# Performance work log

Measured on AMD Instinct MI355X. Metric: run time of the kernel, lower is better.

## Reference

```python
import jax, jax.numpy as jnp
import numpy as np

# ---- dims (from init_kwargs) ----
B_SZ = 16; K = 1; NC = 64; NR = 4; RF = 4; L_UL = 8
M_ANT = 256; N_ANT = 1024; BS_TDD = 16; RIS_TDD = 16
FC = 100e9; BW = 1e9; UPSNR = 10.0; MAX_DELAY = 5e-9; BIT = 1
C = NC  # PSA channel = Nc


def setup_inputs():
    key = jax.random.key(0)
    ks = jax.random.split(key, 20)
    f = jnp.float32
    d = {}
    d['H_BR_re'] = jax.random.normal(ks[0], (NC, N_ANT, M_ANT), f)
    d['H_BR_im'] = jax.random.normal(ks[1], (NC, N_ANT, M_ANT), f)
    d['H_RU_re'] = jax.random.normal(ks[2], (B_SZ, K, NC, NR, N_ANT), f)
    d['H_RU_im'] = jax.random.normal(ks[3], (B_SZ, K, NC, NR, N_ANT), f)
    d['H_BU_re'] = jax.random.normal(ks[4], (B_SZ, K, NC, NR, M_ANT), f)
    d['H_BU_im'] = jax.random.normal(ks[5], (B_SZ, K, NC, NR, M_ANT), f)
    # unit complex Gaussian noise, scaled by sqrt(Power*SNR/2) inside reference
    d['noise_re'] = jax.random.normal(ks[6], (B_SZ, L_UL, NC, NR, RF), f)
    d['noise_im'] = jax.random.normal(ks[7], (B_SZ, L_UL, NC, NR, RF), f)
    # learned parameters (torch: Parameter tensors in __init__)
    d['Phase1'] = jax.random.uniform(ks[8], (L_UL, N_ANT), f)
    d['Phase2'] = jax.random.uniform(ks[9], (L_UL, N_ANT), f)
    d['Phase_TDD'] = jax.random.normal(ks[10], (L_UL, RIS_TDD), f)
    d['S_analog'] = jax.random.normal(ks[11], (L_UL, NC, M_ANT, RF), f)
    d['S_analog_TDD'] = jax.random.normal(ks[12], (L_UL, NC, BS_TDD, RF), f)
    # ParallelPolarizedSelfAttention(channel=Nc) weights (1x1 convs -> [out,in])
    s = 0.05
    d['ch_wv_w'] = jax.random.normal(ks[13], (C // 2, C), f) * s
    d['ch_wv_b'] = jnp.zeros((C // 2,), f)
    d['ch_wq_w'] = jax.random.normal(ks[14], (1, C), f) * s
    d['ch_wq_b'] = jnp.zeros((1,), f)
    d['ch_wz_w'] = jax.random.normal(ks[15], (C, C // 2), f) * s
    d['ch_wz_b'] = jnp.zeros((C,), f)
    d['ln_w'] = jnp.ones((C,), f)
    d['ln_b'] = jnp.zeros((C,), f)
    d['sp_wv_w'] = jax.random.normal(ks[16], (C // 2, C), f) * s
    d['sp_wv_b'] = jnp.zeros((C // 2,), f)
    d['sp_wq_w'] = jax.random.normal(ks[17], (C // 2, C), f) * s
    d['sp_wq_b'] = jnp.zeros((C // 2,), f)
    return d


def _conv1x1(x, w, b):
    # 1x1 conv == channel mixing
    return jnp.einsum('bchw,oc->bohw', x, w) + b[None, :, None, None]


def _psa(x, ch_wv_w, ch_wv_b, ch_wq_w, ch_wq_b, ch_wz_w, ch_wz_b, ln_w, ln_b,
         sp_wv_w, sp_wv_b, sp_wq_w, sp_wq_b):
    # Parallel Polarized Self-Attention (channel branch + spatial branch)
    b, c, h, w = x.shape
    # channel-only self-attention
    cwv = _conv1x1(x, ch_wv_w, ch_wv_b).reshape(b, c // 2, h * w)
    cwq = jax.nn.softmax(_conv1x1(x, ch_wq_w, ch_wq_b).reshape(b, h * w), axis=1)
    cwz = jnp.einsum('bkn,bn->bk', cwv, cwq)          # [b, c//2]
    z = cwz @ ch_wz_w.T + ch_wz_b                      # [b, c]
    mu = jnp.mean(z, axis=-1, keepdims=True)
    var = jnp.var(z, axis=-1, keepdims=True)
    zn = (z - mu) / jnp.sqrt(var + 1e-5) * ln_w + ln_b  # LayerNorm over channel
    ch_weight = jax.nn.sigmoid(zn)[:, :, None, None]
    # spatial-only self-attention
    swv = _conv1x1(x, sp_wv_w, sp_wv_b).reshape(b, c // 2, h * w)
    swq = jax.nn.softmax(jnp.mean(_conv1x1(x, sp_wq_w, sp_wq_b), axis=(2, 3)), axis=-1)
    swz = jnp.einsum('bk,bkn->bn', swq, swv)
    sp_weight = jax.nn.sigmoid(swz.reshape(b, 1, h, w))
    return sp_weight * x + ch_weight * x


def reference(H_BR_re, H_BR_im, H_RU_re, H_RU_im, H_BU_re, H_BU_im,
              noise_re, noise_im, Phase1, Phase2, Phase_TDD, S_analog, S_analog_TDD,
              ch_wv_w, ch_wv_b, ch_wq_w, ch_wq_b, ch_wz_w, ch_wz_b, ln_w, ln_b,
              sp_wv_w, sp_wv_b, sp_wq_w, sp_wq_b):
    H_BR = H_BR_re + 1j * H_BR_im                       # [Nc, N_ant, M_ant]
    H_RU = H_RU_re[:, K - 1] + 1j * H_RU_im[:, K - 1]   # [B, Nc, Nr, N_ant]
    H_BU = H_BU_re[:, K - 1] + 1j * H_BU_im[:, K - 1]   # [B, Nc, Nr, M_ant]
    two_pi = 2.0 * jnp.pi
    # subcarrier frequencies fm = (n - (Nc+1)/2) * B/Nc + fc
    fm = ((jnp.arange(NC, dtype=jnp.float32) + 1.0) - (NC + 1) / 2.0) * (BW / NC) + FC
    # phase quantization (bit = 1 -> seg = pi)
    seg = two_pi / (2 ** BIT)
    th1 = jnp.exp(1j * (jnp.floor(two_pi * Phase1 / seg) * seg))  # [L, N_ant]
    th2 = jnp.exp(1j * (jnp.floor(two_pi * Phase2 / seg) * seg))  # [L, N_ant]
    # RIS true-time-delay phase, kron(Phi_T, ones(1, N_ant//RIS_TDD)) == repeat
    a1 = MAX_DELAY * jax.nn.sigmoid(Phase_TDD)                    # [L, RIS_TDD]
    phi_t = jnp.exp(1j * two_pi * fm[None, :, None] * a1[:, None, :])
    phi_tdd = jnp.repeat(phi_t, N_ANT // RIS_TDD, axis=-1)        # [L, Nc, N_ant]
    theta = th1[:, None, :] * phi_tdd * th2[:, None, :]           # diag(Theta) entries
    # BS analog precoder with TTDs; kron(S_T, ones(M//BS_TDD,1)) == row repeat
    S = jnp.exp(1j * S_analog) / float(np.sqrt(M_ANT))            # [L, Nc, M, RF]
    bdel = MAX_DELAY * jax.nn.sigmoid(S_analog_TDD)               # [L, Nc, BS_TDD, RF]
    s_t = jnp.exp(1j * two_pi * fm[None, :, None, None] * bdel)
    F = S * jnp.repeat(s_t, M_ANT // BS_TDD, axis=2)              # [L, Nc, M, RF]
    # H_RU @ diag(theta) == column-wise scaling (fused, no NxN diag matmul)
    scaled = H_RU[:, None] * theta[None, :, :, None, :]           # [B, L, Nc, Nr, N_ant]
    a = jnp.einsum('blcrn,cnm->blcrm', scaled, H_BR) + H_BU[:, None]
    y0 = jnp.einsum('blcrm,lcmf->blcrf', a, F)                    # [B, L, Nc, Nr, RF]
    power = jnp.sum(jnp.abs(y0) ** 2, axis=(3, 4))[..., None, None]
    snr_lin = 10.0 ** (-UPSNR / 10.0)
    noise = (noise_re + 1j * noise_im) * jnp.sqrt(power * snr_lin / 2.0)
    y = y0 + noise
    Y = jnp.transpose(y, (0, 2, 3, 4, 1)).reshape(B_SZ, NC, K * NR * RF, L_UL)
    x = jnp.concatenate([jnp.real(Y), jnp.imag(Y)], axis=3)       # [B, Nc, K*Nr*RF, 2L]
    return _psa(x, ch_wv_w, ch_wv_b, ch_wq_w, ch_wq_b, ch_wz_w, ch_wz_b,
                ln_w, ln_b, sp_wv_w, sp_wv_b, sp_wq_w, sp_wq_b)
```

## Files before the change

kernel.cpp:

```cpp
#include <hip/hip_runtime.h>
#include <math.h>

static constexpr double TWO_PI_D = 6.283185307179586476925287;

static constexpr size_t OFF_THRE = 0;
static constexpr size_t OFF_THIM = 524288;
static constexpr size_t OFF_FBF  = 1048576;
static constexpr size_t OFF_WTBF = 1572864;
static constexpr size_t OFF_Y0P  = 3670016;
static constexpr size_t OFF_X    = 4980736;
static constexpr size_t WS_FLOATS = 5242880;

typedef __attribute__((ext_vector_type(8))) short short8;
typedef __attribute__((ext_vector_type(4))) float f32x4;
typedef __attribute__((address_space(3))) unsigned int lds_u32;
typedef const __attribute__((address_space(1))) unsigned int glo_u32;

__device__ __forceinline__ double fm_of(int c){
  return ((double)(c + 1) - 32.5) * (1.0e9 / 64.0) + 1.0e11;
}
__device__ __forceinline__ unsigned short f2bf(float x){
  unsigned int u = __float_as_uint(x);
  return (unsigned short)((u + 0x7FFFu + ((u >> 16) & 1u)) >> 16);
}

__global__ __launch_bounds__(256) void k_prep(
    const float* __restrict__ P1, const float* __restrict__ P2,
    const float* __restrict__ PT, const float* __restrict__ SA,
    const float* __restrict__ ST,
    float* __restrict__ tre, float* __restrict__ tim, unsigned short* __restrict__ Fbf)
{
  __shared__ double tcs[16], tsn[16];
  int bid = blockIdx.x, tid = threadIdx.x;
  const float TWO_PI_F = 6.2831855f, SEG_F = 3.1415927f;
  if (bid < 2048){
    int l = bid >> 8, c = (bid >> 2) & 63, n0 = (bid & 3) * 256;
    if (tid < 4){
      int ris = (n0 >> 6) + tid;
      double a1 = 5.0e-9 / (1.0 + exp((double)(-PT[l * 16 + ris])));
      sincos(TWO_PI_D * fm_of(c) * a1, &tsn[tid], &tcs[tid]);
    }
    __syncthreads();
    int n = n0 + tid;
    float p1 = P1[l * 1024 + n], p2 = P2[l * 1024 + n];
    int k1 = (int)floorf((TWO_PI_F * p1) / SEG_F);
    int k2 = (int)floorf((TWO_PI_F * p2) / SEG_F);
    float s = ((k1 + k2) & 1) ? -1.f : 1.f;
    int t = (l * 64 + c) * 1024 + n;
    int ti = tid >> 6;
    tre[t] = s * (float)tcs[ti];
    tim[t] = s * (float)tsn[ti];
  } else {
    int bid2 = bid - 2048;
    int l = bid2 >> 8, c = (bid2 >> 2) & 63, f = bid2 & 3;
    int m = tid;
    if (tid < 16){
      double bdel = 5.0e-9 / (1.0 + exp((double)(-ST[((l * 64 + c) * 16 + tid) * 4 + f])));
      sincos(TWO_PI_D * fm_of(c) * bdel, &tsn[tid], &tcs[tid]);
    }
    __syncthreads();
    float sa_ = SA[(size_t)((l * 64 + c) * 256 + m) * 4 + f];
    float ssa, csa;
    sincosf(sa_, &ssa, &csa);
    float cb = (float)tcs[m >> 4], sb = (float)tsn[m >> 4];
    size_t base = ((size_t)(c * 2) * 32 + (l * 4 + f)) * 256 + m;
    Fbf[base]        = f2bf((csa * cb - ssa * sb) * 0.0625f);
    Fbf[base + 8192] = f2bf((csa * sb + ssa * cb) * 0.0625f);
  }
}

__global__ __launch_bounds__(256, 2) void k_W(
    const float* __restrict__ Hre, const float* __restrict__ Him,
    const unsigned short* __restrict__ Fbf,
    const float* __restrict__ tre, const float* __restrict__ tim,
    unsigned short* __restrict__ WTbf)
{
  __shared__ __align__(16) float lA[16640];
  const int bid = blockIdx.x;
  const int c = bid >> 5;
  const int n0 = (bid & 31) * 32;
  const int tid = threadIdx.x;
  const int lane = tid & 63, w = tid >> 6;

  const float* hre0 = Hre + ((size_t)c * 1024 + n0) * 256;
  const float* him0 = Him + ((size_t)c * 1024 + n0) * 256;
  #pragma unroll
  for (int i = 0; i < 16; i++){
    int t = w * 16 + i;
    int row = t & 31;
    const float* src = ((t >> 5) ? him0 : hre0) + (size_t)row * 256 + (lane << 2);
    __builtin_amdgcn_global_load_lds((glo_u32*)src, (lds_u32*)&lA[t * 260], 16, 0, 0);
  }
  __syncthreads();

  const int lftile = w & 1, rowhalf = w >> 1;
  const int kq = lane >> 4, rm = lane & 15;
  const int lf = lftile * 16 + rm;
  const int rrow = rowhalf * 16 + rm;
  const int nt = n0 + rowhalf * 16;

  const float* aRe = &lA[rrow * 260 + kq * 8];
  const float* aIm = aRe + 32 * 260;
  const unsigned short* fr = Fbf + (size_t)c * 16384 + (size_t)lf * 256 + kq * 8;
  const unsigned short* fi = fr + 8192;

  f32x4 accRe = {0.f,0.f,0.f,0.f}, accIm = {0.f,0.f,0.f,0.f};

  #pragma unroll
  for (int ck = 0; ck < 8; ck++){
    const int mo = ck * 32;
    float4 r0 = *(const float4*)(aRe + mo);
    float4 r1 = *(const float4*)(aRe + mo + 4);
    float4 i0 = *(const float4*)(aIm + mo);
    float4 i1 = *(const float4*)(aIm + mo + 4);
    short8 bre = *(const short8*)(fr + mo);
    short8 bim = *(const short8*)(fi + mo);
    short8 are, aim, bin;
    are[0]=(short)f2bf(r0.x); are[1]=(short)f2bf(r0.y); are[2]=(short)f2bf(r0.z); are[3]=(short)f2bf(r0.w);
    are[4]=(short)f2bf(r1.x); are[5]=(short)f2bf(r1.y); are[6]=(short)f2bf(r1.z); are[7]=(short)f2bf(r1.w);
    aim[0]=(short)f2bf(i0.x); aim[1]=(short)f2bf(i0.y); aim[2]=(short)f2bf(i0.z); aim[3]=(short)f2bf(i0.w);
    aim[4]=(short)f2bf(i1.x); aim[5]=(short)f2bf(i1.y); aim[6]=(short)f2bf(i1.z); aim[7]=(short)f2bf(i1.w);
    #pragma unroll
    for (int j = 0; j < 8; j++) bin[j] = bim[j] ^ (short)0x8000;
    accRe = __builtin_amdgcn_mfma_f32_16x16x32_bf16(are, bre, accRe, 0, 0, 0);
    accRe = __builtin_amdgcn_mfma_f32_16x16x32_bf16(aim, bin, accRe, 0, 0, 0);
    accIm = __builtin_amdgcn_mfma_f32_16x16x32_bf16(are, bim, accIm, 0, 0, 0);
    accIm = __builtin_amdgcn_mfma_f32_16x16x32_bf16(aim, bre, accIm, 0, 0, 0);
  }

  {
    const int l = lf >> 2;
    unsigned short pr[4], pi_[4];
    #pragma unroll
    for (int r = 0; r < 4; r++){
      size_t ti = (size_t)(l * 64 + c) * 1024 + nt + kq * 4 + r;
      float wr = tre[ti], wi = tim[ti];
      float xr = accRe[r], xi = accIm[r];
      pr[r]  = f2bf(wr * xr - wi * xi);
      pi_[r] = f2bf(wr * xi + wi * xr);
    }
    size_t rb = ((size_t)(c * 2) * 32 + lf) * 1024 + nt + kq * 4;
    *(uint2*)(WTbf + rb) =
        make_uint2((unsigned)pr[0] | ((unsigned)pr[1] << 16),
                   (unsigned)pr[2] | ((unsigned)pr[3] << 16));
    *(uint2*)(WTbf + rb + 32768) =
        make_uint2((unsigned)pi_[0] | ((unsigned)pi_[1] << 16),
                   (unsigned)pi_[2] | ((unsigned)pi_[3] << 16));
  }
}

__global__ __launch_bounds__(512) void k_y0(
    const float* __restrict__ Rre, const float* __restrict__ Rim,
    const float* __restrict__ Ure, const float* __restrict__ Uim,
    const unsigned short* __restrict__ WTbf, const unsigned short* __restrict__ Fbf,
    float* __restrict__ Y0p)
{
  __shared__ __align__(16) short lA[2][2][64][32];
  __shared__ __align__(16) short lB[2][2][32][32];
  const int bid = blockIdx.x;
  const int chunk = bid >> 6, c = bid & 63;
  const int tid = threadIdx.x;
  const int lane = tid & 63, w = tid >> 6;
  const int lftile = w & 1, mt = w >> 1;
  const int kq = lane >> 4, rm = lane & 15;
  const int s_mq = tid & 7, s_nr = tid >> 3;
  const int b_comp = tid >> 7, b_lf = (tid >> 2) & 31, b_q = tid & 3;

  const float* Are; const float* Aim; int ars, ac0;
  const unsigned short* Bb; int brs;
  if (chunk < 4){ Are = Rre; Aim = Rim; ars = 1024; ac0 = chunk * 256; Bb = WTbf; brs = 1024; }
  else          { Are = Ure; Aim = Uim; ars = 256;  ac0 = 0;           Bb = Fbf;  brs = 256;  }
  const size_t arow = ((size_t)((s_nr >> 2) * 64 + c) * 4 + (s_nr & 3)) * ars + ac0;

  f32x4 accRe = {0.f,0.f,0.f,0.f}, accIm = {0.f,0.f,0.f,0.f};
  float4 sRe, sIm; short8 sB;

  auto LOADC = [&](int ck){
    size_t g = arow + ck * 32 + s_mq * 4;
    sRe = *(const float4*)(Are + g);
    sIm = *(const float4*)(Aim + g);
    if (tid < 256){
      size_t gb = ((size_t)(c * 2 + b_comp) * 32 + b_lf) * brs + ac0 + ck * 32 + b_q * 8;
      sB = *(const short8*)(Bb + gb);
    }
  };
  auto WRITEC = [&](int buf){
    int eo = (((s_mq >> 1) ^ (s_nr & 3)) << 3) + (s_mq & 1) * 4;
    unsigned int r0 = (unsigned)f2bf(sRe.x) | ((unsigned)f2bf(sRe.y) << 16);
    unsigned int r1 = (unsigned)f2bf(sRe.z) | ((unsigned)f2bf(sRe.w) << 16);
    *(uint2*)&lA[buf][0][s_nr][eo] = make_uint2(r0, r1);
    unsigned int i0 = (unsigned)f2bf(sIm.x) | ((unsigned)f2bf(sIm.y) << 16);
    unsigned int i1 = (unsigned)f2bf(sIm.z) | ((unsigned)f2bf(sIm.w) << 16);
    *(uint2*)&lA[buf][1][s_nr][eo] = make_uint2(i0, i1);
    if (tid < 256){
      *(short8*)&lB[buf][b_comp][b_lf][(b_q ^ (b_lf & 3)) << 3] = sB;
    }
  };
  auto COMPUTE = [&](int buf){
    int col = lftile * 16 + rm;
    int be = (kq ^ (col & 3)) << 3;
    short8 bRe = *(const short8*)&lB[buf][0][col][be];
    short8 bIm = *(const short8*)&lB[buf][1][col][be];
    short8 bImN;
    #pragma unroll
    for (int i = 0; i < 8; i++) bImN[i] = bIm[i] ^ (short)0x8000;
    int row = mt * 16 + rm;
    int eo = (kq ^ (row & 3)) << 3;
    short8 are = *(const short8*)&lA[buf][0][row][eo];
    short8 aim = *(const short8*)&lA[buf][1][row][eo];
    accRe = __builtin_amdgcn_mfma_f32_16x16x32_bf16(are, bRe,  accRe, 0, 0, 0);
    accRe = __builtin_amdgcn_mfma_f32_16x16x32_bf16(aim, bImN, accRe, 0, 0, 0);
    accIm = __builtin_amdgcn_mfma_f32_16x16x32_bf16(are, bIm,  accIm, 0, 0, 0);
    accIm = __builtin_amdgcn_mfma_f32_16x16x32_bf16(aim, bRe,  accIm, 0, 0, 0);
  };

  LOADC(0); WRITEC(0); __syncthreads();
  for (int ck = 0; ck < 8; ck++){
    int buf = ck & 1;
    if (ck < 7) LOADC(ck + 1);
    COMPUTE(buf);
    if (ck < 7) WRITEC(buf ^ 1);
    __syncthreads();
  }

  #pragma unroll
  for (int r = 0; r < 4; r++){
    int row = mt * 16 + kq * 4 + r;
    int lf = lftile * 16 + rm;
    size_t idx = ((size_t)(chunk * 64 + c) * 64 + row) * 32 + lf;
    float2 o; o.x = accRe[r]; o.y = accIm[r];
    *(float2*)(Y0p + idx * 2) = o;
  }
}

__global__ __launch_bounds__(256) void k_fin(
    const float* __restrict__ Y0p,
    const float* __restrict__ nre, const float* __restrict__ nim,
    float* __restrict__ X)
{
  int wid = blockIdx.x * 4 + (threadIdx.x >> 6);
  int lane = threadIdx.x & 63;
  int c = wid & 63, l = (wid >> 6) & 7, b = wid >> 9;
  int pair = lane >> 2;
  int r = pair >> 2, f = pair & 3;
  float yR = 0.f, yI = 0.f;
  #pragma unroll
  for (int ch = 0; ch < 5; ch++){
    size_t idx = ((size_t)(ch * 64 + c) * 64 + b * 4 + r) * 32 + l * 4 + f;
    float2 v = *(const float2*)(Y0p + idx * 2);
    yR += v.x; yI += v.y;
  }
  float p = yR * yR + yI * yI;
  p += __shfl_xor(p, 4); p += __shfl_xor(p, 8);
  p += __shfl_xor(p, 16); p += __shfl_xor(p, 32);
  float sc = sqrtf(p * 0.05f);
  if ((lane & 3) == 0){
    size_t ni = ((size_t)((b * 8 + l) * 64 + c) * 4 + r) * 4 + f;
    float oR = yR + nre[ni] * sc;
    float oI = yI + nim[ni] * sc;
    size_t xb = ((size_t)(b * 64 + c) * 16 + pair) * 16;
    X[xb + l]     = oR;
    X[xb + 8 + l] = oI;
  }
}

__global__ __launch_bounds__(256) void k_psa(
    const float* __restrict__ Xin,
    const float* __restrict__ wv_w, const float* __restrict__ wv_b,
    const float* __restrict__ wq_w, const float* __restrict__ wq_b,
    const float* __restrict__ wz_w, const float* __restrict__ wz_b,
    const float* __restrict__ lnw, const float* __restrict__ lnb,
    const float* __restrict__ sv_w, const float* __restrict__ sv_b,
    const float* __restrict__ sq_w, const float* __restrict__ sq_b,
    float* __restrict__ out)
{
  __shared__ float x[64 * 257];
  __shared__ float buf[256];
  __shared__ float xms[64], xqs[64], chw[64], wcomb[64];
  __shared__ float cwzs[32], swqs[32];
  __shared__ float red4[8];
  int b = blockIdx.x, tid = threadIdx.x;
  const float* xin = Xin + (size_t)b * 16384;
  for (int kk = 0; kk < 64; kk++){
    int i = tid + 256 * kk;
    x[(i >> 8) * 257 + (i & 255)] = xin[i];
  }
  __syncthreads();
  if (tid < 64){
    float s = 0.f;
    for (int n = 0; n < 256; n++) s += x[tid * 257 + n];
    xms[tid] = s * (1.f / 256.f);
  }
  float lq = wq_b[0];
  for (int cc = 0; cc < 64; cc++) lq += wq_w[cc] * x[cc * 257 + tid];
  float mx = lq;
  for (int s = 1; s < 64; s <<= 1) mx = fmaxf(mx, __shfl_xor(mx, s));
  if ((tid & 63) == 0) red4[tid >> 6] = mx;
  __syncthreads();
  mx = fmaxf(fmaxf(red4[0], red4[1]), fmaxf(red4[2], red4[3]));
  float e = expf(lq - mx);
  float se = e;
  for (int s = 1; s < 64; s <<= 1) se += __shfl_xor(se, s);
  if ((tid & 63) == 0) red4[4 + (tid >> 6)] = se;
  __syncthreads();
  se = red4[4] + red4[5] + red4[6] + red4[7];
  buf[tid] = e / se;
  __syncthreads();
  if (tid < 64){
    float s = 0.f;
    for (int n = 0; n < 256; n++) s += x[tid * 257 + n] * buf[n];
    xqs[tid] = s;
  }
  __syncthreads();
  if (tid < 32){
    float s = wv_b[tid];
    for (int cc = 0; cc < 64; cc++) s += wv_w[tid * 64 + cc] * xqs[cc];
    cwzs[tid] = s;
  }
  __syncthreads();
  if (tid < 64){
    float z = wz_b[tid];
    for (int k = 0; k < 32; k++) z += cwzs[k] * wz_w[tid * 32 + k];
    float s1 = z, s2 = z * z;
    for (int s = 1; s < 64; s <<= 1){ s1 += __shfl_xor(s1, s); s2 += __shfl_xor(s2, s); }
    float mu = s1 * (1.f / 64.f);
    float var = s2 * (1.f / 64.f) - mu * mu;
    float zn = (z - mu) * rsqrtf(var + 1e-5f) * lnw[tid] + lnb[tid];
    chw[tid] = 1.f / (1.f + expf(-zn));
  }
  if (tid < 32){
    float s = sq_b[tid];
    for (int cc = 0; cc < 64; cc++) s += sq_w[tid * 64 + cc] * xms[cc];
    float m2 = s;
    for (int st = 1; st < 32; st <<= 1) m2 = fmaxf(m2, __shfl_xor(m2, st));
    float ee = expf(s - m2), ss = ee;
    for (int st = 1; st < 32; st <<= 1) ss += __shfl_xor(ss, st);
    swqs[tid] = ee / ss;
  }
  __syncthreads();
  if (tid < 64){
    float s = 0.f;
    for (int k = 0; k < 32; k++) s += swqs[k] * sv_w[k * 64 + tid];
    wcomb[tid] = s;
  }
  __syncthreads();
  float bcomb = 0.f;
  for (int k = 0; k < 32; k++) bcomb += swqs[k] * sv_b[k];
  float sz = bcomb;
  for (int cc = 0; cc < 64; cc++) sz += wcomb[cc] * x[cc * 257 + tid];
  float spw = 1.f / (1.f + expf(-sz));
  buf[tid] = spw;
  __syncthreads();
  for (int kk = 0; kk < 64; kk++){
    int i = tid + 256 * kk;
    int cc = i >> 8, n = i & 255;
    out[(size_t)b * 16384 + i] = (buf[n] + chw[cc]) * x[cc * 257 + n];
  }
}

extern "C" void kernel_launch(void* const* d_in, const int* in_sizes, int n_in,
                              void* d_out, int out_size, void* d_ws, size_t ws_size,
                              hipStream_t stream)
{
  if (ws_size < WS_FLOATS * sizeof(float)) return;
  const float* HBRre = (const float*)d_in[0];
  const float* HBRim = (const float*)d_in[1];
  const float* HRUre = (const float*)d_in[2];
  const float* HRUim = (const float*)d_in[3];
  const float* HBUre = (const float*)d_in[4];
  const float* HBUim = (const float*)d_in[5];
  const float* nre   = (const float*)d_in[6];
  const float* nim   = (const float*)d_in[7];
  const float* P1    = (const float*)d_in[8];
  const float* P2    = (const float*)d_in[9];
  const float* PT    = (const float*)d_in[10];
  const float* SA    = (const float*)d_in[11];
  const float* ST    = (const float*)d_in[12];
  const float* wv_w  = (const float*)d_in[13];
  const float* wv_b  = (const float*)d_in[14];
  const float* wq_w  = (const float*)d_in[15];
  const float* wq_b  = (const float*)d_in[16];
  const float* wz_w  = (const float*)d_in[17];
  const float* wz_b  = (const float*)d_in[18];
  const float* lnw   = (const float*)d_in[19];
  const float* lnb   = (const float*)d_in[20];
  const float* sv_w  = (const float*)d_in[21];
  const float* sv_b  = (const float*)d_in[22];
  const float* sq_w  = (const float*)d_in[23];
  const float* sq_b  = (const float*)d_in[24];

  float* ws  = (float*)d_ws;
  float* tre = ws + OFF_THRE;
  float* tim = ws + OFF_THIM;
  unsigned short* fbf  = (unsigned short*)(ws + OFF_FBF);
  unsigned short* wtbf = (unsigned short*)(ws + OFF_WTBF);
  float* y0p = ws + OFF_Y0P;
  float* xb  = ws + OFF_X;

  k_prep<<<4096, 256, 0, stream>>>(P1, P2, PT, SA, ST, tre, tim, fbf);
  k_W<<<2048, 256, 0, stream>>>(HBRre, HBRim, fbf, tre, tim, wtbf);
  k_y0<<<320, 512, 0, stream>>>(HRUre, HRUim, HBUre, HBUim, wtbf, fbf, y0p);
  k_fin<<<2048, 256, 0, stream>>>(y0p, nre, nim, xb);
  k_psa<<<16, 256, 0, stream>>>(xb, wv_w, wv_b, wq_w, wq_b, wz_w, wz_b,
                                lnw, lnb, sv_w, sv_b, sq_w, sq_b, (float*)d_out);
}
```

Baseline: 72.09 us.

## Double-buffer H_BR slabs in k_W with register-resident F and theta

k_W now gives each block four 32-row chunks of H_BR (512 blocks instead of 2048). While one chunk is computed, the next is loaded into a second LDS buffer with async global_load_lds, and explicit vmcnt waits and barriers keep the two in step. The F fragments and theta values are loaded into registers once per block and reused across chunks. The LDS layout switches from padding to an XOR swizzle to avoid bank conflicts. In exchange the kernel uses more LDS and registers (launch bounds set to one block per CU) and exposes less parallelism across blocks.

Measured after the change: 70.32 us. 1.03x faster.

```diff
diff --git a/kernel.cpp b/kernel.cpp
--- a/kernel.cpp
+++ b/kernel.cpp
@@ -69,84 +69,113 @@
   }
 }
 
-__global__ __launch_bounds__(256, 2) void k_W(
+#define WAITV16 asm volatile("s_waitcnt vmcnt(16)" ::: "memory")
+#define WAITV0  asm volatile("s_waitcnt vmcnt(0)" ::: "memory")
+#define SBAR    __builtin_amdgcn_s_barrier()
+
+__global__ __launch_bounds__(256, 1) void k_W(
     const float* __restrict__ Hre, const float* __restrict__ Him,
     const unsigned short* __restrict__ Fbf,
     const float* __restrict__ tre, const float* __restrict__ tim,
     unsigned short* __restrict__ WTbf)
 {
-  __shared__ __align__(16) float lA[16640];
+  __shared__ __align__(16) float lA[2][2][32][256];
   const int bid = blockIdx.x;
-  const int c = bid >> 5;
-  const int n0 = (bid & 31) * 32;
+  const int c = bid >> 3;
+  const int slab0 = (bid & 7) * 128;
   const int tid = threadIdx.x;
   const int lane = tid & 63, w = tid >> 6;
-
-  const float* hre0 = Hre + ((size_t)c * 1024 + n0) * 256;
-  const float* him0 = Him + ((size_t)c * 1024 + n0) * 256;
-  #pragma unroll
-  for (int i = 0; i < 16; i++){
-    int t = w * 16 + i;
-    int row = t & 31;
-    const float* src = ((t >> 5) ? him0 : hre0) + (size_t)row * 256 + (lane << 2);
-    __builtin_amdgcn_global_load_lds((glo_u32*)src, (lds_u32*)&lA[t * 260], 16, 0, 0);
-  }
-  __syncthreads();
-
   const int lftile = w & 1, rowhalf = w >> 1;
   const int kq = lane >> 4, rm = lane & 15;
   const int lf = lftile * 16 + rm;
-  const int rrow = rowhalf * 16 + rm;
-  const int nt = n0 + rowhalf * 16;
-
-  const float* aRe = &lA[rrow * 260 + kq * 8];
-  const float* aIm = aRe + 32 * 260;
-  const unsigned short* fr = Fbf + (size_t)c * 16384 + (size_t)lf * 256 + kq * 8;
-  const unsigned short* fi = fr + 8192;
-
-  f32x4 accRe = {0.f,0.f,0.f,0.f}, accIm = {0.f,0.f,0.f,0.f};
-
+  const int l = lf >> 2;
+
+  const unsigned short* frp = Fbf + (size_t)c * 16384 + (size_t)lf * 256 + kq * 8;
+  short8 Fre[8], Fim[8];
   #pragma unroll
-  for (int ck = 0; ck < 8; ck++){
-    const int mo = ck * 32;
-    float4 r0 = *(const float4*)(aRe + mo);
-    float4 r1 = *(const float4*)(aRe + mo + 4);
-    float4 i0 = *(const float4*)(aIm + mo);
-    float4 i1 = *(const float4*)(aIm + mo + 4);
-    short8 bre = *(const short8*)(fr + mo);
-    short8 bim = *(const short8*)(fi + mo);
-    short8 are, aim, bin;
-    are[0]=(short)f2bf(r0.x); are[1]=(short)f2bf(r0.y); are[2]=(short)f2bf(r0.z); are[3]=(short)f2bf(r0.w);
-    are[4]=(short)f2bf(r1.x); are[5]=(short)f2bf(r1.y); are[6]=(short)f2bf(r1.z); are[7]=(short)f2bf(r1.w);
-    aim[0]=(short)f2bf(i0.x); aim[1]=(short)f2bf(i0.y); aim[2]=(short)f2bf(i0.z); aim[3]=(short)f2bf(i0.w);
-    aim[4]=(short)f2bf(i1.x); aim[5]=(short)f2bf(i1.y); aim[6]=(short)f2bf(i1.z); aim[7]=(short)f2bf(i1.w);
+  for (int k = 0; k < 8; k++){
+    Fre[k] = *(const short8*)(frp + k * 32);
+    Fim[k] = *(const short8*)(frp + 8192 + k * 32);
+  }
+  float thR[16], thI[16];
+  {
+    size_t tb = (size_t)(l * 64 + c) * 1024 + slab0 + rowhalf * 16 + kq * 4;
     #pragma unroll
-    for (int j = 0; j < 8; j++) bin[j] = bim[j] ^ (short)0x8000;
-    accRe = __builtin_amdgcn_mfma_f32_16x16x32_bf16(are, bre, accRe, 0, 0, 0);
-    accRe = __builtin_amdgcn_mfma_f32_16x16x32_bf16(aim, bin, accRe, 0, 0, 0);
-    accIm = __builtin_amdgcn_mfma_f32_16x16x32_bf16(are, bim, accIm, 0, 0, 0);
-    accIm = __builtin_amdgcn_mfma_f32_16x16x32_bf16(aim, bre, accIm, 0, 0, 0);
-  }
-
-  {
-    const int l = lf >> 2;
+    for (int ch = 0; ch < 4; ch++){
+      #pragma unroll
+      for (int r = 0; r < 4; r++){
+        thR[ch * 4 + r] = tre[tb + ch * 32 + r];
+        thI[ch * 4 + r] = tim[tb + ch * 32 + r];
+      }
+    }
+  }
+
+  const float* hre0 = Hre + ((size_t)c * 1024 + slab0) * 256;
+  const float* him0 = Him + ((size_t)c * 1024 + slab0) * 256;
+
+  auto STAGE = [&](int ch){
+    #pragma unroll
+    for (int i = 0; i < 16; i++){
+      int t = w * 16 + i;
+      int comp = t >> 5;
+      int row = t & 31;
+      const float* src = (comp ? him0 : hre0) + ((size_t)(ch * 32 + row)) * 256
+                         + ((lane ^ (row & 7)) << 2);
+      __builtin_amdgcn_global_load_lds((glo_u32*)src,
+          (lds_u32*)&lA[ch & 1][comp][row][0], 16, 0, 0);
+    }
+  };
+
+  auto COMP = [&](int ch){
+    f32x4 accRe = {0.f,0.f,0.f,0.f}, accIm = {0.f,0.f,0.f,0.f};
+    const float* bre = &lA[ch & 1][0][0][0];
+    const float* bim = &lA[ch & 1][1][0][0];
+    const int row = rowhalf * 16 + rm;
+    const int rb = row * 256;
+    const int s4 = (row & 7) << 4;
+    #pragma unroll
+    for (int ck = 0; ck < 8; ck++){
+      int x0 = ck * 128 + kq * 32;
+      int i0 = (x0 ^ s4) >> 2;
+      int i1 = ((x0 + 16) ^ s4) >> 2;
+      float4 r0 = *(const float4*)(bre + rb + i0);
+      float4 r1 = *(const float4*)(bre + rb + i1);
+      float4 m0 = *(const float4*)(bim + rb + i0);
+      float4 m1 = *(const float4*)(bim + rb + i1);
+      short8 are, aim, bin;
+      are[0]=(short)f2bf(r0.x); are[1]=(short)f2bf(r0.y); are[2]=(short)f2bf(r0.z); are[3]=(short)f2bf(r0.w);
+      are[4]=(short)f2bf(r1.x); are[5]=(short)f2bf(r1.y); are[6]=(short)f2bf(r1.z); are[7]=(short)f2bf(r1.w);
+      aim[0]=(short)f2bf(m0.x); aim[1]=(short)f2bf(m0.y); aim[2]=(short)f2bf(m0.z); aim[3]=(short)f2bf(m0.w);
+      aim[4]=(short)f2bf(m1.x); aim[5]=(short)f2bf(m1.y); aim[6]=(short)f2bf(m1.z); aim[7]=(short)f2bf(m1.w);
+      #pragma unroll
+      for (int j = 0; j < 8; j++) bin[j] = Fim[ck][j] ^ (short)0x8000;
+      accRe = __builtin_amdgcn_mfma_f32_16x16x32_bf16(are, Fre[ck], accRe, 0, 0, 0);
+      accRe = __builtin_amdgcn_mfma_f32_16x16x32_bf16(aim, bin,     accRe, 0, 0, 0);
+      accIm = __builtin_amdgcn_mfma_f32_16x16x32_bf16(are, Fim[ck], accIm, 0, 0, 0);
+      accIm = __builtin_amdgcn_mfma_f32_16x16x32_bf16(aim, Fre[ck], accIm, 0, 0, 0);
+    }
     unsigned short pr[4], pi_[4];
     #pragma unroll
     for (int r = 0; r < 4; r++){
-      size_t ti = (size_t)(l * 64 + c) * 1024 + nt + kq * 4 + r;
-      float wr = tre[ti], wi = tim[ti];
+      float wr = thR[ch * 4 + r], wi = thI[ch * 4 + r];
       float xr = accRe[r], xi = accIm[r];
       pr[r]  = f2bf(wr * xr - wi * xi);
       pi_[r] = f2bf(wr * xi + wi * xr);
     }
-    size_t rb = ((size_t)(c * 2) * 32 + lf) * 1024 + nt + kq * 4;
-    *(uint2*)(WTbf + rb) =
+    size_t rb2 = ((size_t)(c * 2) * 32 + lf) * 1024 + slab0 + ch * 32 + rowhalf * 16 + kq * 4;
+    *(uint2*)(WTbf + rb2) =
         make_uint2((unsigned)pr[0] | ((unsigned)pr[1] << 16),
                    (unsigned)pr[2] | ((unsigned)pr[3] << 16));
-    *(uint2*)(WTbf + rb + 32768) =
+    *(uint2*)(WTbf + rb2 + 32768) =
         make_uint2((unsigned)pi_[0] | ((unsigned)pi_[1] << 16),
                    (unsigned)pi_[2] | ((unsigned)pi_[3] << 16));
-  }
+  };
+
+  STAGE(0);
+  STAGE(1); WAITV16; SBAR; COMP(0); SBAR;
+  STAGE(2); WAITV16; SBAR; COMP(1); SBAR;
+  STAGE(3); WAITV16; SBAR; COMP(2); SBAR;
+  WAITV0;            SBAR; COMP(3);
 }
 
 __global__ __launch_bounds__(512) void k_y0(
@@ -398,7 +427,7 @@
   float* xb  = ws + OFF_X;
 
   k_prep<<<4096, 256, 0, stream>>>(P1, P2, PT, SA, ST, tre, tim, fbf);
-  k_W<<<2048, 256, 0, stream>>>(HBRre, HBRim, fbf, tre, tim, wtbf);
+  k_W<<<512, 256, 0, stream>>>(HBRre, HBRim, fbf, tre, tim, wtbf);
   k_y0<<<320, 512, 0, stream>>>(HRUre, HRUim, HBUre, HBUim, wtbf, fbf, y0p);
   k_fin<<<2048, 256, 0, stream>>>(y0p, nre, nim, xb);
   k_psa<<<16, 256, 0, stream>>>(xb, wv_w, wv_b, wq_w, wq_b, wz_w, wz_b,
```
